# Performance work log

Measured on AMD Instinct MI355X. Metric: run time of the kernel, lower is better.

## Reference

```python
import jax, jax.numpy as jnp
import numpy as np

B, T, NMELS = 512, 180, 40
HID, NLAYER, PROJ = 768, 3, 256


def _lstm_layer(x, w_ih, w_hh, b):
    """PyTorch-convention LSTM layer. x: [B, T, D] -> h_seq: [B, T, H].
    Gate order i, f, g, o. b = b_ih + b_hh."""
    Bn = x.shape[0]
    H = w_hh.shape[1]
    # Input contribution for all timesteps at once: [T, B, 4H]
    xg = jnp.einsum('btd,gd->tbg', x, w_ih) + b

    def step(carry, xg_t):
        h, c = carry
        g = xg_t + h @ w_hh.T  # [B, 4H]
        i, f, gg, o = jnp.split(g, 4, axis=-1)
        i = jax.nn.sigmoid(i)
        f = jax.nn.sigmoid(f)
        gg = jnp.tanh(gg)
        o = jax.nn.sigmoid(o)
        c = f * c + i * gg
        h = o * jnp.tanh(c)
        return (h, c), h

    h0 = jnp.zeros((Bn, H), x.dtype)
    c0 = jnp.zeros((Bn, H), x.dtype)
    (_, _), hs = jax.lax.scan(step, (h0, c0), xg)  # hs: [T, B, H]
    return jnp.transpose(hs, (1, 0, 2))


def setup_inputs() -> dict:
    key = jax.random.key(0)
    ks = jax.random.split(key, 16)
    G = 4 * HID

    def xavier(k, shape):
        fan_out, fan_in = shape
        std = np.sqrt(2.0 / (fan_in + fan_out)).astype(np.float32)
        return jax.random.normal(k, shape, jnp.float32) * std

    inp = {
        'x': jax.random.normal(ks[0], (B, T, NMELS), jnp.float32),
        'w_ih0': xavier(ks[1], (G, NMELS)),
        'w_hh0': xavier(ks[2], (G, HID)),
        'b_ih0': jnp.zeros((G,), jnp.float32),
        'b_hh0': jnp.zeros((G,), jnp.float32),
        'w_ih1': xavier(ks[3], (G, HID)),
        'w_hh1': xavier(ks[4], (G, HID)),
        'b_ih1': jnp.zeros((G,), jnp.float32),
        'b_hh1': jnp.zeros((G,), jnp.float32),
        'w_ih2': xavier(ks[5], (G, HID)),
        'w_hh2': xavier(ks[6], (G, HID)),
        'b_ih2': jnp.zeros((G,), jnp.float32),
        'b_hh2': jnp.zeros((G,), jnp.float32),
        'proj_w': xavier(ks[7], (PROJ, HID)),
        'proj_b': jnp.zeros((PROJ,), jnp.float32),
    }
    return inp


def reference(x, w_ih0, w_hh0, b_ih0, b_hh0,
              w_ih1, w_hh1, b_ih1, b_hh1,
              w_ih2, w_hh2, b_ih2, b_hh2,
              proj_w, proj_b):
    h = _lstm_layer(x, w_ih0, w_hh0, b_ih0 + b_hh0)
    h = _lstm_layer(h, w_ih1, w_hh1, b_ih1 + b_hh1)
    h = _lstm_layer(h, w_ih2, w_hh2, b_ih2 + b_hh2)
    last = h[:, -1]                       # [B, HID] last timestep
    e = last @ proj_w.T + proj_b          # [B, PROJ]
    e = e / jnp.linalg.norm(e, axis=1, keepdims=True)
    return e
```

## Files before the change

kernel.cpp:

```cpp
#include <hip/hip_runtime.h>
#include <cstdint>
#include <cstddef>

using u16 = unsigned short;
using u32 = unsigned int;

typedef __attribute__((ext_vector_type(8)))  __bf16 bf16x8;
typedef __attribute__((ext_vector_type(16))) float  f32x16;

constexpr int kB   = 512;
constexpr int kT   = 180;
constexpr int kH   = 768;
constexpr int NBLK = 192;

constexpr int L0N  = 16 * 192 * 832;
constexpr int L12N = 16 * 192 * 1536;

constexpr int RING_SLOT_E = 24 * 512 * 32;
constexpr size_t RING_SZ  = (size_t)2 * RING_SLOT_E * 2;

constexpr size_t OFF_R0  = 256;
constexpr size_t OFF_R1  = OFF_R0 + RING_SZ;
constexpr size_t OFF_R2  = OFF_R1 + RING_SZ;
constexpr size_t OFF_PB  = OFF_R2 + RING_SZ;
constexpr size_t OFF_XT  = OFF_PB + (size_t)3 * 3072 * 4;
constexpr size_t OFF_W0  = OFF_XT + (size_t)kT * kB * 64 * 2;
constexpr size_t OFF_W1  = OFF_W0 + (size_t)L0N * 2;
constexpr size_t OFF_W2  = OFF_W1 + (size_t)L12N * 2;
constexpr size_t WS_NEED = OFF_W2 + (size_t)L12N * 2;

#define CLB __asm__ volatile("" ::: "memory")

__device__ __forceinline__ float bf2f(u16 u) {
  union { u32 i; float f; } v; v.i = ((u32)u) << 16; return v.f;
}
__device__ __forceinline__ u16 f2bf(float f) {
  union { float f; u32 i; } v; v.f = f;
  u32 r = v.i + 0x7fffu + ((v.i >> 16) & 1u);
  return (u16)(r >> 16);
}

typedef __attribute__((address_space(1))) const u32 as1_u32;
typedef __attribute__((address_space(3))) u32 as3_u32;
__device__ __forceinline__ void gload_lds16(const u16* g, u16* l) {
  __builtin_amdgcn_global_load_lds((as1_u32*)g, (as3_u32*)l, 16, 0, 0);
}
__device__ __forceinline__ void gload_lds16_dc(const u16* g, u16* l) {
  __builtin_amdgcn_global_load_lds((as1_u32*)g, (as3_u32*)l, 16, 0, 16);
}

__global__ void k_zero(uint4* p, int n) {
  uint4 z = make_uint4(0u, 0u, 0u, 0u);
  for (int i = blockIdx.x * 256 + threadIdx.x; i < n; i += gridDim.x * 256) p[i] = z;
}

__global__ void k_pack_w(const float* __restrict__ wih0, const float* __restrict__ whh0,
                         const float* __restrict__ wih1, const float* __restrict__ whh1,
                         const float* __restrict__ wih2, const float* __restrict__ whh2,
                         u16* __restrict__ W0, u16* __restrict__ W1, u16* __restrict__ W2) {
  int idx = blockIdx.x * 256 + threadIdx.x;
  if (idx < L0N) {
    int col = idx / 832, k = idx - col * 832;
    int ntile = col / 192, p = col - ntile * 192;
    int g = p / 48, hc = p - g * 48;
    int gcol = g * 768 + ntile * 48 + hc;
    float v = (k < 40) ? wih0[gcol * 40 + k]
                       : ((k < 64) ? 0.f : whh0[(size_t)gcol * 768 + (k - 64)]);
    W0[idx] = f2bf(v);
  } else if (idx < L0N + L12N) {
    int li = idx - L0N;
    int col = li / 1536, k = li - col * 1536;
    int ntile = col / 192, p = col - ntile * 192;
    int g = p / 48, hc = p - g * 48;
    int gcol = g * 768 + ntile * 48 + hc;
    float v = (k < 768) ? wih1[(size_t)gcol * 768 + k] : whh1[(size_t)gcol * 768 + (k - 768)];
    W1[li] = f2bf(v);
  } else {
    int li = idx - (L0N + L12N);
    if (li < L12N) {
      int col = li / 1536, k = li - col * 1536;
      int ntile = col / 192, p = col - ntile * 192;
      int g = p / 48, hc = p - g * 48;
      int gcol = g * 768 + ntile * 48 + hc;
      float v = (k < 768) ? wih2[(size_t)gcol * 768 + k] : whh2[(size_t)gcol * 768 + (k - 768)];
      W2[li] = f2bf(v);
    }
  }
}

__global__ void k_pack_b(const float* __restrict__ bi0, const float* __restrict__ bh0,
                         const float* __restrict__ bi1, const float* __restrict__ bh1,
                         const float* __restrict__ bi2, const float* __restrict__ bh2,
                         float* __restrict__ pbo) {
  int idx = blockIdx.x * 256 + threadIdx.x;
  int l = idx / 3072, r = idx - l * 3072;
  int ntile = r / 192, p = r - ntile * 192;
  int g = p / 48, hc = p - g * 48;
  int gcol = g * 768 + ntile * 48 + hc;
  const float* bi = (l == 0) ? bi0 : ((l == 1) ? bi1 : bi2);
  const float* bh = (l == 0) ? bh0 : ((l == 1) ? bh1 : bh2);
  pbo[idx] = bi[gcol] + bh[gcol];
}

__global__ void k_xT(const float* __restrict__ x, u16* __restrict__ xT) {
  int idx = blockIdx.x * 256 + threadIdx.x;
  int t = idx / (512 * 64);
  int r = idx - t * 512 * 64;
  int b = r >> 6, j = r & 63;
  float v = (j < 40) ? x[((size_t)b * 180 + t) * 40 + j] : 0.f;
  xT[(size_t)t * 32768 + (size_t)(j >> 5) * 16384 + b * 32 + (j & 31)] = f2bf(v);
}

__global__ __launch_bounds__(256, 2) void k_lstm(
    const u16* __restrict__ xT,
    u16* __restrict__ ring0, u16* __restrict__ ring1, u16* __restrict__ ring2,
    const u16* __restrict__ W0, const u16* __restrict__ W1, const u16* __restrict__ W2,
    const float* __restrict__ pb, u32* __restrict__ bar) {
  __shared__ __align__(16) unsigned char smem[61440 + 768];
  u16*   scr = (u16*)smem;
  float* pbs = (float*)(smem + 61440);

  const int tid = threadIdx.x;
  const int bid = blockIdx.x;
  const int xcd = bid & 7, j0 = bid >> 3;
  const int g_    = (j0 >> 2) * 8 + xcd;
  const int mt    = j0 & 3;
  const int layer = g_ >> 4;
  const int ntile = g_ & 15;
  const int mrow0 = mt * 128;

  const u16* Wl     = (layer == 0) ? W0 : ((layer == 1) ? W1 : W2);
  const int  Kl     = (layer == 0) ? 832 : 1536;
  const int  KcIn   = (layer == 0) ? 2 : 24;
  const int  nch    = (layer == 0) ? 26 : 48;
  const u16* inseq  = (layer == 1) ? ring0 : ring1;
  u16*       ringS  = (layer == 0) ? ring0 : ((layer == 1) ? ring1 : ring2);
  const u16* bbase0 = Wl + (size_t)(ntile * 192) * Kl;

  for (int i = tid; i < 192; i += 256) pbs[i] = pb[layer * 3072 + ntile * 192 + i];

  const int wid = tid >> 6, lane = tid & 63;
  const int wm = wid & 1, wn = wid >> 1;
  const int l31 = lane & 31, lhi = lane >> 5;

  float c_reg[24];
#pragma unroll
  for (int i = 0; i < 24; i++) c_reg[i] = 0.f;

  for (int s = 0; s < kT + 2; ++s) {
    const int t = s - layer;
    if (t >= 0 && t < kT) {
      f32x16 acc[2][3];
#pragma unroll
      for (int mi = 0; mi < 2; mi++)
#pragma unroll
        for (int ni = 0; ni < 3; ni++)
#pragma unroll
          for (int r = 0; r < 16; r++) acc[mi][ni][r] = 0.f;

      const u16* inbase  = (layer == 0) ? (xT + (size_t)t * 32768)
                                        : (inseq + (size_t)(t & 1) * RING_SLOT_E);
      const u16* recbase = ringS + (size_t)((t - 1) & 1) * RING_SLOT_E;

      auto stage = [&](int c, int st) {
        u16* sbA = (u16*)(smem + st * 20480);
        u16* sbB = sbA + 4096;
        const bool rsrc = (layer != 0) || (c >= KcIn);
        const u16* abase = (c < KcIn) ? (inbase + (size_t)c * 16384)
                                      : (recbase + (size_t)(c - KcIn) * 16384);
#pragma unroll
        for (int k = 0; k < 2; k++) {
          const int e = tid + k * 256;
          const int row = e >> 2, sp = e & 3;
          const int so = sp ^ ((row >> 1) & 3);
          const u16* ga = abase + (size_t)(mrow0 + row) * 32 + so * 8;
          u16*       la = sbA + (size_t)e * 8;
          if (rsrc) gload_lds16_dc(ga, la);
          else      gload_lds16(ga, la);
        }
        const u16* bb = bbase0 + c * 32;
#pragma unroll
        for (int k = 0; k < 3; k++) {
          const int e = tid + k * 256;
          const int col = e >> 2, sp = e & 3;
          const int so = sp ^ ((col >> 1) & 3);
          gload_lds16(bb + (size_t)col * Kl + so * 8, sbB + (size_t)e * 8);
        }
      };

      stage(0, 0);
      stage(1, 1);
      for (int c = 0; c < nch; ++c) {
        CLB;
        if (c == nch - 1) __builtin_amdgcn_s_waitcnt(0xF70);
        else              __builtin_amdgcn_s_waitcnt(0xF75);
        __builtin_amdgcn_s_barrier();
        CLB;
        if (c + 2 < nch) stage(c + 2, (c + 2) % 3);
        const u16* sA = (const u16*)(smem + (c % 3) * 20480);
        const u16* sB = sA + 4096;
        const int wsw = (l31 >> 1) & 3;
#pragma unroll
        for (int kk = 0; kk < 2; kk++) {
          const int sl = (((kk << 1) | lhi) ^ wsw) << 3;
          bf16x8 a0 = *(const bf16x8*)(sA + (wm * 64 +      l31) * 32 + sl);
          bf16x8 a1 = *(const bf16x8*)(sA + (wm * 64 + 32 + l31) * 32 + sl);
          const int c0 = wn * 96 + l31;
          bf16x8 b0 = *(const bf16x8*)(sB + (c0     ) * 32 + sl);
          bf16x8 b1 = *(const bf16x8*)(sB + (c0 + 32) * 32 + sl);
          bf16x8 b2 = *(const bf16x8*)(sB + (c0 + 64) * 32 + sl);
          acc[0][0] = __builtin_amdgcn_mfma_f32_32x32x16_bf16(a0, b0, acc[0][0], 0, 0, 0);
          acc[0][1] = __builtin_amdgcn_mfma_f32_32x32x16_bf16(a0, b1, acc[0][1], 0, 0, 0);
          acc[0][2] = __builtin_amdgcn_mfma_f32_32x32x16_bf16(a0, b2, acc[0][2], 0, 0, 0);
          acc[1][0] = __builtin_amdgcn_mfma_f32_32x32x16_bf16(a1, b0, acc[1][0], 0, 0, 0);
          acc[1][1] = __builtin_amdgcn_mfma_f32_32x32x16_bf16(a1, b1, acc[1][1], 0, 0, 0);
          acc[1][2] = __builtin_amdgcn_mfma_f32_32x32x16_bf16(a1, b2, acc[1][2], 0, 0, 0);
        }
      }
      __syncthreads();
#pragma unroll
      for (int mi = 0; mi < 2; mi++) {
#pragma unroll
        for (int ni = 0; ni < 3; ni++) {
          const int pcol = wn * 96 + ni * 32 + l31;
          const int gg = pcol / 48;
          const float bias = pbs[pcol];
#pragma unroll
          for (int r = 0; r < 16; r++) {
            const int rowl = wm * 64 + mi * 32 + (r & 3) + ((r >> 2) << 3) + (lhi << 2);
            float v = acc[mi][ni][r] + bias;
            v = (gg == 2) ? tanhf(v) : (1.f / (1.f + __expf(-v)));
            scr[rowl * 192 + pcol] = f2bf(v);
          }
        }
      }
      __syncthreads();
      u16* hout = ringS + (size_t)(t & 1) * RING_SLOT_E;
#pragma unroll
      for (int jj = 0; jj < 24; jj++) {
        const int idx = jj * 256 + tid;
        const int row = idx / 48;
        const int hc  = idx - row * 48;
        const float iv = bf2f(scr[row * 192       + hc]);
        const float fv = bf2f(scr[row * 192 +  48 + hc]);
        const float gv = bf2f(scr[row * 192 +  96 + hc]);
        const float ov = bf2f(scr[row * 192 + 144 + hc]);
        const float cn = fv * c_reg[jj] + iv * gv;
        c_reg[jj] = cn;
        const int colg = ntile * 48 + hc;
        hout[(size_t)(colg >> 5) * 16384 + (size_t)(mrow0 + row) * 32 + (colg & 31)]
            = f2bf(ov * tanhf(cn));
      }
    }
    __syncthreads();
    if (tid == 0) {
      __hip_atomic_fetch_add(bar, 1u, __ATOMIC_RELEASE, __HIP_MEMORY_SCOPE_AGENT);
      const u32 goal = (u32)(s + 1) * (u32)NBLK;
      u32 tries = 0;
      while (__hip_atomic_load(bar, __ATOMIC_RELAXED, __HIP_MEMORY_SCOPE_AGENT) < goal) {
        __builtin_amdgcn_s_sleep(8);
        if (++tries > 100000u) break;
      }
    }
    __syncthreads();
  }
}

__global__ __launch_bounds__(256) void k_proj(const u16* __restrict__ hlast,
                                              const float* __restrict__ pw,
                                              const float* __restrict__ pbv,
                                              float* __restrict__ out) {
  __shared__ float hs[8 * 768];
  __shared__ float wred[4 * 8];
  __shared__ float inv[8];
  const int tid = threadIdx.x;
  const int r0 = blockIdx.x * 8;
  for (int i = tid; i < 8 * 768; i += 256) {
    const int b = i / 768, col = i - b * 768;
    hs[i] = bf2f(hlast[(size_t)(col >> 5) * 16384 + (size_t)(r0 + b) * 32 + (col & 31)]);
  }
  __syncthreads();
  float acc[8];
#pragma unroll
  for (int r = 0; r < 8; r++) acc[r] = 0.f;
  const float* wrow = pw + (size_t)tid * 768;
  for (int k = 0; k < 768; k++) {
    float w = wrow[k];
#pragma unroll
    for (int r = 0; r < 8; r++) acc[r] += hs[r * 768 + k] * w;
  }
  const float bv = pbv[tid];
#pragma unroll
  for (int r = 0; r < 8; r++) acc[r] += bv;
  const int lane = tid & 63, w4 = tid >> 6;
#pragma unroll
  for (int r = 0; r < 8; r++) {
    float v = acc[r] * acc[r];
#pragma unroll
    for (int off = 32; off > 0; off >>= 1) v += __shfl_xor(v, off);
    if (lane == 0) wred[w4 * 8 + r] = v;
  }
  __syncthreads();
  if (tid < 8) {
    float sum = wred[tid] + wred[8 + tid] + wred[16 + tid] + wred[24 + tid];
    inv[tid] = 1.f / sqrtf(sum);
  }
  __syncthreads();
#pragma unroll
  for (int r = 0; r < 8; r++) out[(size_t)(r0 + r) * 256 + tid] = acc[r] * inv[r];
}

extern "C" void kernel_launch(void* const* d_in, const int* in_sizes, int n_in,
                              void* d_out, int out_size, void* d_ws, size_t ws_size,
                              hipStream_t stream) {
  const float* x    = (const float*)d_in[0];
  const float* wih0 = (const float*)d_in[1];
  const float* whh0 = (const float*)d_in[2];
  const float* bi0  = (const float*)d_in[3];
  const float* bh0  = (const float*)d_in[4];
  const float* wih1 = (const float*)d_in[5];
  const float* whh1 = (const float*)d_in[6];
  const float* bi1  = (const float*)d_in[7];
  const float* bh1  = (const float*)d_in[8];
  const float* wih2 = (const float*)d_in[9];
  const float* whh2 = (const float*)d_in[10];
  const float* bi2  = (const float*)d_in[11];
  const float* bh2  = (const float*)d_in[12];
  const float* pw   = (const float*)d_in[13];
  const float* pbv  = (const float*)d_in[14];

  if (ws_size < WS_NEED) return;

  char* ws  = (char*)d_ws;
  u32*  bar = (u32*)(ws + 0);
  u16*  r0  = (u16*)(ws + OFF_R0);
  u16*  r1  = (u16*)(ws + OFF_R1);
  u16*  r2  = (u16*)(ws + OFF_R2);
  float* pb = (float*)(ws + OFF_PB);
  u16*  xT  = (u16*)(ws + OFF_XT);
  u16*  W0  = (u16*)(ws + OFF_W0);
  u16*  W1  = (u16*)(ws + OFF_W1);
  u16*  W2  = (u16*)(ws + OFF_W2);

  hipLaunchKernelGGL(k_zero, dim3(512), dim3(256), 0, stream,
                     (uint4*)ws, (int)(OFF_PB / 16));
  hipLaunchKernelGGL(k_pack_w, dim3((L0N + 2 * L12N + 255) / 256), dim3(256), 0, stream,
                     wih0, whh0, wih1, whh1, wih2, whh2, W0, W1, W2);
  hipLaunchKernelGGL(k_pack_b, dim3(36), dim3(256), 0, stream,
                     bi0, bh0, bi1, bh1, bi2, bh2, pb);
  hipLaunchKernelGGL(k_xT, dim3(kT * kB * 64 / 256), dim3(256), 0, stream, x, xT);

  {
    const u16* xTc = xT; const float* pbc = pb;
    const u16 *W0c = W0, *W1c = W1, *W2c = W2;
    u16 *r0m = r0, *r1m = r1, *r2m = r2; u32* barm = bar;
    void* kargs[] = {(void*)&xTc, (void*)&r0m, (void*)&r1m, (void*)&r2m,
                     (void*)&W0c, (void*)&W1c, (void*)&W2c, (void*)&pbc, (void*)&barm};
    hipLaunchCooperativeKernel((void*)k_lstm, dim3(NBLK), dim3(256), kargs, 0, stream);
  }

  hipLaunchKernelGGL(k_proj, dim3(64), dim3(256), 0, stream,
                     r2 + (size_t)((kT - 1) & 1) * RING_SLOT_E, pw, pbv, (float*)d_out);
}
```

Measured before the change: 9.341 ms.

## Replace global grid barrier with per-row-tile dataflow flags and wider blocks

Halves the block count to 96 with 512 threads each, so every block now computes a 384-column gate tile and the weights are repacked to match. The single grid-wide barrier per step is replaced by per-(layer, row-tile) counters. Each block waits only on its input layer, its own previous step and the next layer's consumption of the ring slot. The LDS pipeline moves to four dynamic-shared-memory stages of 32 KB, and biases are held in registers. The aim is to cut global barrier latency and let layers run in a wavefront, at the cost of more LDS per block, fewer blocks and subtler ordering correctness.

Measured after the change: 9.980 ms. 6.8% more time.

```diff
diff --git a/kernel.cpp b/kernel.cpp
--- a/kernel.cpp
+++ b/kernel.cpp
@@ -11,15 +11,16 @@
 constexpr int kB   = 512;
 constexpr int kT   = 180;
 constexpr int kH   = 768;
-constexpr int NBLK = 192;
-
-constexpr int L0N  = 16 * 192 * 832;
-constexpr int L12N = 16 * 192 * 1536;
+constexpr int NBLK = 96;
+constexpr int NTHR = 512;
+
+constexpr int L0N  = 8 * 384 * 832;
+constexpr int L12N = 8 * 384 * 1536;
 
 constexpr int RING_SLOT_E = 24 * 512 * 32;
 constexpr size_t RING_SZ  = (size_t)2 * RING_SLOT_E * 2;
 
-constexpr size_t OFF_R0  = 256;
+constexpr size_t OFF_R0  = 4096;
 constexpr size_t OFF_R1  = OFF_R0 + RING_SZ;
 constexpr size_t OFF_R2  = OFF_R1 + RING_SZ;
 constexpr size_t OFF_PB  = OFF_R2 + RING_SZ;
@@ -29,6 +30,10 @@
 constexpr size_t OFF_W2  = OFF_W1 + (size_t)L12N * 2;
 constexpr size_t WS_NEED = OFF_W2 + (size_t)L12N * 2;
 
+constexpr size_t STAGE_SZ = 32768;
+constexpr int    NSTG     = 4;
+constexpr size_t DYN_LDS  = NSTG * STAGE_SZ;
+
 #define CLB __asm__ volatile("" ::: "memory")
 
 __device__ __forceinline__ float bf2f(u16 u) {
@@ -61,27 +66,27 @@
   int idx = blockIdx.x * 256 + threadIdx.x;
   if (idx < L0N) {
     int col = idx / 832, k = idx - col * 832;
-    int ntile = col / 192, p = col - ntile * 192;
-    int g = p / 48, hc = p - g * 48;
-    int gcol = g * 768 + ntile * 48 + hc;
+    int ntile = col / 384, p = col - ntile * 384;
+    int g = p / 96, hc = p - g * 96;
+    int gcol = g * 768 + ntile * 96 + hc;
     float v = (k < 40) ? wih0[gcol * 40 + k]
                        : ((k < 64) ? 0.f : whh0[(size_t)gcol * 768 + (k - 64)]);
     W0[idx] = f2bf(v);
   } else if (idx < L0N + L12N) {
     int li = idx - L0N;
     int col = li / 1536, k = li - col * 1536;
-    int ntile = col / 192, p = col - ntile * 192;
-    int g = p / 48, hc = p - g * 48;
-    int gcol = g * 768 + ntile * 48 + hc;
+    int ntile = col / 384, p = col - ntile * 384;
+    int g = p / 96, hc = p - g * 96;
+    int gcol = g * 768 + ntile * 96 + hc;
     float v = (k < 768) ? wih1[(size_t)gcol * 768 + k] : whh1[(size_t)gcol * 768 + (k - 768)];
     W1[li] = f2bf(v);
   } else {
     int li = idx - (L0N + L12N);
     if (li < L12N) {
       int col = li / 1536, k = li - col * 1536;
-      int ntile = col / 192, p = col - ntile * 192;
-      int g = p / 48, hc = p - g * 48;
-      int gcol = g * 768 + ntile * 48 + hc;
+      int ntile = col / 384, p = col - ntile * 384;
+      int g = p / 96, hc = p - g * 96;
+      int gcol = g * 768 + ntile * 96 + hc;
       float v = (k < 768) ? wih2[(size_t)gcol * 768 + k] : whh2[(size_t)gcol * 768 + (k - 768)];
       W2[li] = f2bf(v);
     }
@@ -94,9 +99,9 @@
                          float* __restrict__ pbo) {
   int idx = blockIdx.x * 256 + threadIdx.x;
   int l = idx / 3072, r = idx - l * 3072;
-  int ntile = r / 192, p = r - ntile * 192;
-  int g = p / 48, hc = p - g * 48;
-  int gcol = g * 768 + ntile * 48 + hc;
+  int ntile = r / 384, p = r - ntile * 384;
+  int g = p / 96, hc = p - g * 96;
+  int gcol = g * 768 + ntile * 96 + hc;
   const float* bi = (l == 0) ? bi0 : ((l == 1) ? bi1 : bi2);
   const float* bh = (l == 0) ? bh0 : ((l == 1) ? bh1 : bh2);
   pbo[idx] = bi[gcol] + bh[gcol];
@@ -111,22 +116,20 @@
   xT[(size_t)t * 32768 + (size_t)(j >> 5) * 16384 + b * 32 + (j & 31)] = f2bf(v);
 }
 
-__global__ __launch_bounds__(256, 2) void k_lstm(
+__global__ __launch_bounds__(512, 2) void k_lstm(
     const u16* __restrict__ xT,
     u16* __restrict__ ring0, u16* __restrict__ ring1, u16* __restrict__ ring2,
     const u16* __restrict__ W0, const u16* __restrict__ W1, const u16* __restrict__ W2,
-    const float* __restrict__ pb, u32* __restrict__ bar) {
-  __shared__ __align__(16) unsigned char smem[61440 + 768];
-  u16*   scr = (u16*)smem;
-  float* pbs = (float*)(smem + 61440);
+    const float* __restrict__ pb, u32* __restrict__ flg) {
+  extern __shared__ __align__(16) unsigned char smem[];
+  u16* scr = (u16*)smem;
 
   const int tid = threadIdx.x;
   const int bid = blockIdx.x;
-  const int xcd = bid & 7, j0 = bid >> 3;
-  const int g_    = (j0 >> 2) * 8 + xcd;
+  const int ntile = bid & 7;
+  const int j0    = bid >> 3;
+  const int layer = j0 >> 2;
   const int mt    = j0 & 3;
-  const int layer = g_ >> 4;
-  const int ntile = g_ & 15;
   const int mrow0 = mt * 128;
 
   const u16* Wl     = (layer == 0) ? W0 : ((layer == 1) ? W1 : W2);
@@ -135,134 +138,145 @@
   const int  nch    = (layer == 0) ? 26 : 48;
   const u16* inseq  = (layer == 1) ? ring0 : ring1;
   u16*       ringS  = (layer == 0) ? ring0 : ((layer == 1) ? ring1 : ring2);
-  const u16* bbase0 = Wl + (size_t)(ntile * 192) * Kl;
-
-  for (int i = tid; i < 192; i += 256) pbs[i] = pb[layer * 3072 + ntile * 192 + i];
+  const u16* bbase0 = Wl + (size_t)(ntile * 384) * Kl;
+
+  u32* Fself = flg + (size_t)((layer * 4 + mt) * 64);
+  u32* Fin   = flg + (size_t)(((layer - 1) * 4 + mt) * 64);
+  u32* Fnxt  = flg + (size_t)(((layer + 1) * 4 + mt) * 64);
 
   const int wid = tid >> 6, lane = tid & 63;
   const int wm = wid & 1, wn = wid >> 1;
   const int l31 = lane & 31, lhi = lane >> 5;
 
+  float bias_r[3];
+#pragma unroll
+  for (int ni = 0; ni < 3; ni++)
+    bias_r[ni] = pb[layer * 3072 + ntile * 384 + wn * 96 + ni * 32 + l31];
+
   float c_reg[24];
 #pragma unroll
   for (int i = 0; i < 24; i++) c_reg[i] = 0.f;
 
-  for (int s = 0; s < kT + 2; ++s) {
-    const int t = s - layer;
-    if (t >= 0 && t < kT) {
-      f32x16 acc[2][3];
-#pragma unroll
-      for (int mi = 0; mi < 2; mi++)
-#pragma unroll
-        for (int ni = 0; ni < 3; ni++)
-#pragma unroll
-          for (int r = 0; r < 16; r++) acc[mi][ni][r] = 0.f;
-
-      const u16* inbase  = (layer == 0) ? (xT + (size_t)t * 32768)
-                                        : (inseq + (size_t)(t & 1) * RING_SLOT_E);
-      const u16* recbase = ringS + (size_t)((t - 1) & 1) * RING_SLOT_E;
-
-      auto stage = [&](int c, int st) {
-        u16* sbA = (u16*)(smem + st * 20480);
-        u16* sbB = sbA + 4096;
-        const bool rsrc = (layer != 0) || (c >= KcIn);
-        const u16* abase = (c < KcIn) ? (inbase + (size_t)c * 16384)
-                                      : (recbase + (size_t)(c - KcIn) * 16384);
-#pragma unroll
-        for (int k = 0; k < 2; k++) {
-          const int e = tid + k * 256;
-          const int row = e >> 2, sp = e & 3;
-          const int so = sp ^ ((row >> 1) & 3);
-          const u16* ga = abase + (size_t)(mrow0 + row) * 32 + so * 8;
-          u16*       la = sbA + (size_t)e * 8;
-          if (rsrc) gload_lds16_dc(ga, la);
-          else      gload_lds16(ga, la);
-        }
-        const u16* bb = bbase0 + c * 32;
-#pragma unroll
-        for (int k = 0; k < 3; k++) {
-          const int e = tid + k * 256;
-          const int col = e >> 2, sp = e & 3;
-          const int so = sp ^ ((col >> 1) & 3);
-          gload_lds16(bb + (size_t)col * Kl + so * 8, sbB + (size_t)e * 8);
+  for (int t = 0; t < kT; ++t) {
+    if (tid == 0) {
+      auto spinf = [&](u32* f, u32 goal) {
+        u32 tries = 0;
+        while (__hip_atomic_load(f, __ATOMIC_RELAXED, __HIP_MEMORY_SCOPE_AGENT) < goal) {
+          __builtin_amdgcn_s_sleep(4);
+          if (++tries > 400000u) break;
         }
       };
-
-      stage(0, 0);
-      stage(1, 1);
-      for (int c = 0; c < nch; ++c) {
-        CLB;
-        if (c == nch - 1) __builtin_amdgcn_s_waitcnt(0xF70);
-        else              __builtin_amdgcn_s_waitcnt(0xF75);
-        __builtin_amdgcn_s_barrier();
-        CLB;
-        if (c + 2 < nch) stage(c + 2, (c + 2) % 3);
-        const u16* sA = (const u16*)(smem + (c % 3) * 20480);
-        const u16* sB = sA + 4096;
-        const int wsw = (l31 >> 1) & 3;
-#pragma unroll
-        for (int kk = 0; kk < 2; kk++) {
-          const int sl = (((kk << 1) | lhi) ^ wsw) << 3;
-          bf16x8 a0 = *(const bf16x8*)(sA + (wm * 64 +      l31) * 32 + sl);
-          bf16x8 a1 = *(const bf16x8*)(sA + (wm * 64 + 32 + l31) * 32 + sl);
-          const int c0 = wn * 96 + l31;
-          bf16x8 b0 = *(const bf16x8*)(sB + (c0     ) * 32 + sl);
-          bf16x8 b1 = *(const bf16x8*)(sB + (c0 + 32) * 32 + sl);
-          bf16x8 b2 = *(const bf16x8*)(sB + (c0 + 64) * 32 + sl);
-          acc[0][0] = __builtin_amdgcn_mfma_f32_32x32x16_bf16(a0, b0, acc[0][0], 0, 0, 0);
-          acc[0][1] = __builtin_amdgcn_mfma_f32_32x32x16_bf16(a0, b1, acc[0][1], 0, 0, 0);
-          acc[0][2] = __builtin_amdgcn_mfma_f32_32x32x16_bf16(a0, b2, acc[0][2], 0, 0, 0);
-          acc[1][0] = __builtin_amdgcn_mfma_f32_32x32x16_bf16(a1, b0, acc[1][0], 0, 0, 0);
-          acc[1][1] = __builtin_amdgcn_mfma_f32_32x32x16_bf16(a1, b1, acc[1][1], 0, 0, 0);
-          acc[1][2] = __builtin_amdgcn_mfma_f32_32x32x16_bf16(a1, b2, acc[1][2], 0, 0, 0);
+      if (layer >= 1)           spinf(Fin,   8u * (u32)(t + 1));
+      if (t >= 1)               spinf(Fself, 8u * (u32)t);
+      if (layer <= 1 && t >= 2) spinf(Fnxt,  8u * (u32)(t - 1));
+    }
+    __syncthreads();
+
+    f32x16 acc[2][3];
+#pragma unroll
+    for (int mi = 0; mi < 2; mi++)
+#pragma unroll
+      for (int ni = 0; ni < 3; ni++)
+#pragma unroll
+        for (int r = 0; r < 16; r++) acc[mi][ni][r] = 0.f;
+
+    const u16* inbase  = (layer == 0) ? (xT + (size_t)t * 32768)
+                                      : (inseq + (size_t)(t & 1) * RING_SLOT_E);
+    const u16* recbase = ringS + (size_t)((t - 1) & 1) * RING_SLOT_E;
+
+    auto stage = [&](int c, int st) {
+      u16* sbA = (u16*)(smem + (size_t)st * STAGE_SZ);
+      u16* sbB = sbA + 4096;
+      const bool rsrc = (layer != 0) || (c >= KcIn);
+      const u16* abase = (c < KcIn) ? (inbase + (size_t)c * 16384)
+                                    : (recbase + (size_t)(c - KcIn) * 16384);
+      {
+        const int e = tid;
+        const int row = e >> 2, sp = e & 3;
+        const int so = sp ^ ((row >> 1) & 3);
+        const u16* ga = abase + (size_t)(mrow0 + row) * 32 + so * 8;
+        u16*       la = sbA + (size_t)e * 8;
+        if (rsrc) gload_lds16_dc(ga, la);
+        else      gload_lds16(ga, la);
+      }
+      const u16* bb = bbase0 + c * 32;
+#pragma unroll
+      for (int k = 0; k < 3; k++) {
+        const int e = tid + k * 512;
+        const int col = e >> 2, sp = e & 3;
+        const int so = sp ^ ((col >> 1) & 3);
+        gload_lds16(bb + (size_t)col * Kl + so * 8, sbB + (size_t)e * 8);
+      }
+    };
+
+    stage(0, 0);
+    stage(1, 1);
+    stage(2, 2);
+    for (int c = 0; c < nch; ++c) {
+      CLB;
+      const int rem = nch - 1 - c;
+      if      (rem >= 2) __builtin_amdgcn_s_waitcnt(0x0F78);
+      else if (rem == 1) __builtin_amdgcn_s_waitcnt(0x0F74);
+      else               __builtin_amdgcn_s_waitcnt(0x0F70);
+      __builtin_amdgcn_s_barrier();
+      CLB;
+      if (c + 3 < nch) stage(c + 3, (c + 3) & 3);
+      const u16* sA = (const u16*)(smem + (size_t)(c & 3) * STAGE_SZ);
+      const u16* sB = sA + 4096;
+      const int wsw = (l31 >> 1) & 3;
+#pragma unroll
+      for (int kk = 0; kk < 2; kk++) {
+        const int sl = (((kk << 1) | lhi) ^ wsw) << 3;
+        bf16x8 a0 = *(const bf16x8*)(sA + (wm * 64 +      l31) * 32 + sl);
+        bf16x8 a1 = *(const bf16x8*)(sA + (wm * 64 + 32 + l31) * 32 + sl);
+        const int c0 = wn * 96 + l31;
+        bf16x8 b0 = *(const bf16x8*)(sB + (c0     ) * 32 + sl);
+        bf16x8 b1 = *(const bf16x8*)(sB + (c0 + 32) * 32 + sl);
+        bf16x8 b2 = *(const bf16x8*)(sB + (c0 + 64) * 32 + sl);
+        acc[0][0] = __builtin_amdgcn_mfma_f32_32x32x16_bf16(a0, b0, acc[0][0], 0, 0, 0);
+        acc[0][1] = __builtin_amdgcn_mfma_f32_32x32x16_bf16(a0, b1, acc[0][1], 0, 0, 0);
+        acc[0][2] = __builtin_amdgcn_mfma_f32_32x32x16_bf16(a0, b2, acc[0][2], 0, 0, 0);
+        acc[1][0] = __builtin_amdgcn_mfma_f32_32x32x16_bf16(a1, b0, acc[1][0], 0, 0, 0);
+        acc[1][1] = __builtin_amdgcn_mfma_f32_32x32x16_bf16(a1, b1, acc[1][1], 0, 0, 0);
+        acc[1][2] = __builtin_amdgcn_mfma_f32_32x32x16_bf16(a1, b2, acc[1][2], 0, 0, 0);
+      }
+    }
+    __syncthreads();
+#pragma unroll
+    for (int mi = 0; mi < 2; mi++) {
+#pragma unroll
+      for (int ni = 0; ni < 3; ni++) {
+        const int pcol = wn * 96 + ni * 32 + l31;
+        const float bias = bias_r[ni];
+#pragma unroll
+        for (int r = 0; r < 16; r++) {
+          const int rowl = wm * 64 + mi * 32 + (r & 3) + ((r >> 2) << 3) + (lhi << 2);
+          float v = acc[mi][ni][r] + bias;
+          v = (wn == 2) ? tanhf(v) : (1.f / (1.f + __expf(-v)));
+          scr[rowl * 384 + pcol] = f2bf(v);
         }
       }
-      __syncthreads();
-#pragma unroll
-      for (int mi = 0; mi < 2; mi++) {
-#pragma unroll
-        for (int ni = 0; ni < 3; ni++) {
-          const int pcol = wn * 96 + ni * 32 + l31;
-          const int gg = pcol / 48;
-          const float bias = pbs[pcol];
-#pragma unroll
-          for (int r = 0; r < 16; r++) {
-            const int rowl = wm * 64 + mi * 32 + (r & 3) + ((r >> 2) << 3) + (lhi << 2);
-            float v = acc[mi][ni][r] + bias;
-            v = (gg == 2) ? tanhf(v) : (1.f / (1.f + __expf(-v)));
-            scr[rowl * 192 + pcol] = f2bf(v);
-          }
-        }
-      }
-      __syncthreads();
-      u16* hout = ringS + (size_t)(t & 1) * RING_SLOT_E;
-#pragma unroll
-      for (int jj = 0; jj < 24; jj++) {
-        const int idx = jj * 256 + tid;
-        const int row = idx / 48;
-        const int hc  = idx - row * 48;
-        const float iv = bf2f(scr[row * 192       + hc]);
-        const float fv = bf2f(scr[row * 192 +  48 + hc]);
-        const float gv = bf2f(scr[row * 192 +  96 + hc]);
-        const float ov = bf2f(scr[row * 192 + 144 + hc]);
-        const float cn = fv * c_reg[jj] + iv * gv;
-        c_reg[jj] = cn;
-        const int colg = ntile * 48 + hc;
-        hout[(size_t)(colg >> 5) * 16384 + (size_t)(mrow0 + row) * 32 + (colg & 31)]
-            = f2bf(ov * tanhf(cn));
-      }
     }
     __syncthreads();
-    if (tid == 0) {
-      __hip_atomic_fetch_add(bar, 1u, __ATOMIC_RELEASE, __HIP_MEMORY_SCOPE_AGENT);
-      const u32 goal = (u32)(s + 1) * (u32)NBLK;
-      u32 tries = 0;
-      while (__hip_atomic_load(bar, __ATOMIC_RELAXED, __HIP_MEMORY_SCOPE_AGENT) < goal) {
-        __builtin_amdgcn_s_sleep(8);
-        if (++tries > 100000u) break;
-      }
+    u16* hout = ringS + (size_t)(t & 1) * RING_SLOT_E;
+#pragma unroll
+    for (int jj = 0; jj < 24; jj++) {
+      const int idx = jj * 512 + tid;
+      const int row = idx / 96;
+      const int hc  = idx - row * 96;
+      const float iv = bf2f(scr[row * 384       + hc]);
+      const float fv = bf2f(scr[row * 384 +  96 + hc]);
+      const float gv = bf2f(scr[row * 384 + 192 + hc]);
+      const float ov = bf2f(scr[row * 384 + 288 + hc]);
+      const float cn = fv * c_reg[jj] + iv * gv;
+      c_reg[jj] = cn;
+      const int colg = ntile * 96 + hc;
+      hout[(size_t)(colg >> 5) * 16384 + (size_t)(mrow0 + row) * 32 + (colg & 31)]
+          = f2bf(ov * tanhf(cn));
     }
     __syncthreads();
+    if (tid == 0)
+      __hip_atomic_fetch_add(Fself, 1u, __ATOMIC_RELEASE, __HIP_MEMORY_SCOPE_AGENT);
   }
 }
 
@@ -331,8 +345,16 @@
 
   if (ws_size < WS_NEED) return;
 
+  static bool attr_done = false;
+  if (!attr_done) {
+    (void)hipFuncSetAttribute((const void*)k_lstm,
+                              hipFuncAttributeMaxDynamicSharedMemorySize,
+                              (int)DYN_LDS);
+    attr_done = true;
+  }
+
   char* ws  = (char*)d_ws;
-  u32*  bar = (u32*)(ws + 0);
+  u32*  flg = (u32*)(ws + 0);
   u16*  r0  = (u16*)(ws + OFF_R0);
   u16*  r1  = (u16*)(ws + OFF_R1);
   u16*  r2  = (u16*)(ws + OFF_R2);
@@ -353,10 +375,11 @@
   {
     const u16* xTc = xT; const float* pbc = pb;
     const u16 *W0c = W0, *W1c = W1, *W2c = W2;
-    u16 *r0m = r0, *r1m = r1, *r2m = r2; u32* barm = bar;
+    u16 *r0m = r0, *r1m = r1, *r2m = r2; u32* flgm = flg;
     void* kargs[] = {(void*)&xTc, (void*)&r0m, (void*)&r1m, (void*)&r2m,
-                     (void*)&W0c, (void*)&W1c, (void*)&W2c, (void*)&pbc, (void*)&barm};
-    hipLaunchCooperativeKernel((void*)k_lstm, dim3(NBLK), dim3(256), kargs, 0, stream);
+                     (void*)&W0c, (void*)&W1c, (void*)&W2c, (void*)&pbc, (void*)&flgm};
+    hipLaunchCooperativeKernel((void*)k_lstm, dim3(NBLK), dim3(NTHR), kargs,
+                               (unsigned int)DYN_LDS, stream);
   }
 
   hipLaunchKernelGGL(k_proj, dim3(64), dim3(256), 0, stream,
```

## Add row-sliced LSTM kernel with per-group flags replacing global grid barrier

Applied to the files above, without the earlier changes.

Adds a new persistent LSTM kernel using 256 blocks. Each block owns a 32-row batch slice and one gate tile, is pinned to its XCD through the hardware XCC id, and runs all three layers in sequence. The single global barrier per wavefront step is replaced by per-slice, per-layer counters, so only the 16 blocks that share rows wait on each other, and layers can pipeline across timesteps. The K loop uses a 6-stage LDS pipeline with split-K across waves and an LDS reduction. The old kernel is kept as a fallback when the device has fewer than 256 CUs or the launch fails. The risks are more serial layer work per block and the extra overhead of flag spinning.

Result: no change. 9.382 ms (+0.4%).

```diff
diff --git a/kernel.cpp b/kernel.cpp
--- a/kernel.cpp
+++ b/kernel.cpp
@@ -11,7 +11,8 @@
 constexpr int kB   = 512;
 constexpr int kT   = 180;
 constexpr int kH   = 768;
-constexpr int NBLK = 192;
+constexpr int NBLK_RS = 256;
+constexpr int NBLK_FB = 192;
 
 constexpr int L0N  = 16 * 192 * 832;
 constexpr int L12N = 16 * 192 * 1536;
@@ -19,7 +20,7 @@
 constexpr int RING_SLOT_E = 24 * 512 * 32;
 constexpr size_t RING_SZ  = (size_t)2 * RING_SLOT_E * 2;
 
-constexpr size_t OFF_R0  = 256;
+constexpr size_t OFF_R0  = 16384;
 constexpr size_t OFF_R1  = OFF_R0 + RING_SZ;
 constexpr size_t OFF_R2  = OFF_R1 + RING_SZ;
 constexpr size_t OFF_PB  = OFF_R2 + RING_SZ;
@@ -29,6 +30,10 @@
 constexpr size_t OFF_W2  = OFF_W1 + (size_t)L12N * 2;
 constexpr size_t WS_NEED = OFF_W2 + (size_t)L12N * 2;
 
+constexpr size_t STAGE_SZ = 14336;
+constexpr int    NSTG     = 6;
+constexpr size_t DYN_LDS  = NSTG * STAGE_SZ;
+
 #define CLB __asm__ volatile("" ::: "memory")
 
 __device__ __forceinline__ float bf2f(u16 u) {
@@ -44,6 +49,9 @@
 typedef __attribute__((address_space(3))) u32 as3_u32;
 __device__ __forceinline__ void gload_lds16(const u16* g, u16* l) {
   __builtin_amdgcn_global_load_lds((as1_u32*)g, (as3_u32*)l, 16, 0, 0);
+}
+__device__ __forceinline__ void gload_lds16_l2(const u16* g, u16* l) {
+  __builtin_amdgcn_global_load_lds((as1_u32*)g, (as3_u32*)l, 16, 0, 1);
 }
 __device__ __forceinline__ void gload_lds16_dc(const u16* g, u16* l) {
   __builtin_amdgcn_global_load_lds((as1_u32*)g, (as3_u32*)l, 16, 0, 16);
@@ -111,7 +119,198 @@
   xT[(size_t)t * 32768 + (size_t)(j >> 5) * 16384 + b * 32 + (j & 31)] = f2bf(v);
 }
 
-__global__ __launch_bounds__(256, 2) void k_lstm(
+__global__ __launch_bounds__(256, 1) void k_lstm_rs(
+    const u16* __restrict__ xT,
+    u16* __restrict__ ring0, u16* __restrict__ ring1, u16* __restrict__ ring2,
+    const u16* __restrict__ W0, const u16* __restrict__ W1, const u16* __restrict__ W2,
+    const float* __restrict__ pb, u32* __restrict__ flg) {
+  extern __shared__ __align__(16) unsigned char smem[];
+  float* red  = (float*)smem;
+  u16*   scr2 = (u16*)(smem + 24576);
+  __shared__ u32 meta[2];
+
+  const int tid = threadIdx.x;
+  if (tid == 0) {
+    u32 xcc;
+    asm volatile("s_getreg_b32 %0, hwreg(HW_REG_XCC_ID)" : "=s"(xcc));
+    xcc &= 7u;
+    u32* xcnt = flg + 3072;
+    u32 slot = __hip_atomic_fetch_add(&xcnt[xcc], 1u, __ATOMIC_RELAXED,
+                                      __HIP_MEMORY_SCOPE_AGENT);
+    meta[0] = xcc; meta[1] = slot & 31u;
+  }
+  __syncthreads();
+  const int xcc = (int)meta[0];
+  const int rs  = (int)(meta[1] >> 4);
+  const int nt  = (int)(meta[1] & 15u);
+  const int r0  = xcc * 64 + rs * 32;
+
+  const int wid = tid >> 6, lane = tid & 63;
+  const int wn2 = wid & 1, kkw = wid >> 1;
+  const int l31 = lane & 31, lhi = lane >> 5;
+
+  u32* F0 = flg + (size_t)(((xcc * 2 + rs) * 3 + 0) * 64);
+  u32* F1 = F0 + 64;
+  u32* F2 = F0 + 128;
+
+  auto spinf = [&](u32* f, u32 goal) {
+    u32 tries = 0;
+    while (__hip_atomic_load(f, __ATOMIC_RELAXED, __HIP_MEMORY_SCOPE_AGENT) < goal) {
+      __builtin_amdgcn_s_sleep(4);
+      if (++tries > 400000u) break;
+    }
+  };
+
+  float bias_r[3][3];
+#pragma unroll
+  for (int l = 0; l < 3; l++)
+#pragma unroll
+    for (int j = 0; j < 3; j++)
+      bias_r[l][j] = pb[l * 3072 + nt * 192 + wn2 * 96 + j * 32 + l31];
+
+  float cst[3][6];
+#pragma unroll
+  for (int l = 0; l < 3; l++)
+#pragma unroll
+    for (int j = 0; j < 6; j++) cst[l][j] = 0.f;
+
+  for (int t = 0; t < kT; ++t) {
+#pragma unroll
+    for (int l = 0; l < 3; ++l) {
+      const u16* Wl   = (l == 0) ? W0 : ((l == 1) ? W1 : W2);
+      const int  Kl   = (l == 0) ? 832 : 1536;
+      const int  KcIn = (l == 0) ? 2 : 24;
+      const int  nch  = (l == 0) ? 26 : 48;
+      u16* ringL = (l == 0) ? ring0 : ((l == 1) ? ring1 : ring2);
+      const u16* inb  = (l == 0) ? (xT + (size_t)t * 32768)
+                                 : (((l == 1) ? ring0 : ring1) + (size_t)(t & 1) * RING_SLOT_E);
+      const u16* recb = ringL + (size_t)((t - 1) & 1) * RING_SLOT_E;
+      const u16* bb0  = Wl + (size_t)(nt * 192) * Kl;
+      u32* Fl = (l == 0) ? F0 : ((l == 1) ? F1 : F2);
+
+      if (tid == 0) {
+        if (l == 0) {
+          if (t >= 1) spinf(F0, 16u * (u32)t);
+          if (t >= 2) spinf(F1, 16u * (u32)(t - 1));
+        } else if (l == 1) {
+          spinf(F0, 16u * (u32)(t + 1));
+          if (t >= 1) spinf(F1, 16u * (u32)t);
+          if (t >= 2) spinf(F2, 16u * (u32)(t - 1));
+        } else {
+          spinf(F1, 16u * (u32)(t + 1));
+          if (t >= 1) spinf(F2, 16u * (u32)t);
+        }
+      }
+      __syncthreads();
+
+      f32x16 acc[3];
+#pragma unroll
+      for (int j = 0; j < 3; j++)
+#pragma unroll
+        for (int r = 0; r < 16; r++) acc[j][r] = 0.f;
+
+      auto stage = [&](int c, int st) {
+        u16* sbA = (u16*)(smem + (size_t)st * STAGE_SZ);
+        u16* sbB = sbA + 1024;
+        const bool rsrc = (l != 0) || (c >= KcIn);
+        const u16* abase = (c < KcIn) ? (inb + (size_t)c * 16384)
+                                      : (recb + (size_t)(c - KcIn) * 16384);
+        if (lane < 32) {
+          const int e = (wid << 5) | lane;
+          const int row = e >> 2, sp = e & 3;
+          const int so = sp ^ ((row >> 1) & 3);
+          const u16* ga = abase + (size_t)(r0 + row) * 32 + so * 8;
+          u16*       la = sbA + (size_t)e * 8;
+          if (rsrc) gload_lds16_l2(ga, la);
+          else      gload_lds16(ga, la);
+        }
+        const u16* bb = bb0 + c * 32;
+#pragma unroll
+        for (int k = 0; k < 3; k++) {
+          const int e = wid * 192 + (k << 6) + lane;
+          const int col = e >> 2, sp = e & 3;
+          const int so = sp ^ ((col >> 1) & 3);
+          gload_lds16(bb + (size_t)col * Kl + so * 8, sbB + (size_t)e * 8);
+        }
+      };
+
+      stage(0, 0); stage(1, 1); stage(2, 2); stage(3, 3); stage(4, 4);
+      for (int c = 0; c < nch; ++c) {
+        CLB;
+        const int rem = nch - 1 - c;
+        switch (rem > 3 ? 4 : rem) {
+          case 0:  __builtin_amdgcn_s_waitcnt(0x0F70); break;
+          case 1:  __builtin_amdgcn_s_waitcnt(0x0F74); break;
+          case 2:  __builtin_amdgcn_s_waitcnt(0x0F78); break;
+          case 3:  __builtin_amdgcn_s_waitcnt(0x0F7C); break;
+          default: __builtin_amdgcn_s_waitcnt(0x4F70); break;
+        }
+        __builtin_amdgcn_s_barrier();
+        CLB;
+        if (c + 5 < nch) stage(c + 5, (c + 5) % NSTG);
+        const u16* sA = (const u16*)(smem + (size_t)(c % NSTG) * STAGE_SZ);
+        const u16* sB = sA + 1024;
+        const int wsw = (l31 >> 1) & 3;
+        const int sl = (((kkw << 1) | lhi) ^ wsw) << 3;
+        bf16x8 a  = *(const bf16x8*)(sA + l31 * 32 + sl);
+        const int c0 = wn2 * 96 + l31;
+        bf16x8 b0 = *(const bf16x8*)(sB + (c0     ) * 32 + sl);
+        bf16x8 b1 = *(const bf16x8*)(sB + (c0 + 32) * 32 + sl);
+        bf16x8 b2 = *(const bf16x8*)(sB + (c0 + 64) * 32 + sl);
+        acc[0] = __builtin_amdgcn_mfma_f32_32x32x16_bf16(a, b0, acc[0], 0, 0, 0);
+        acc[1] = __builtin_amdgcn_mfma_f32_32x32x16_bf16(a, b1, acc[1], 0, 0, 0);
+        acc[2] = __builtin_amdgcn_mfma_f32_32x32x16_bf16(a, b2, acc[2], 0, 0, 0);
+      }
+      __syncthreads();
+
+      if (kkw == 1) {
+#pragma unroll
+        for (int j = 0; j < 3; j++)
+#pragma unroll
+          for (int r = 0; r < 16; r++)
+            red[(size_t)((wn2 * 3 + j) * 16 + r) * 64 + lane] = acc[j][r];
+      }
+      __syncthreads();
+      if (kkw == 0) {
+#pragma unroll
+        for (int j = 0; j < 3; j++) {
+          const int pcol = wn2 * 96 + j * 32 + l31;
+          const int gate = pcol / 48;
+          const float bias = bias_r[l][j];
+#pragma unroll
+          for (int r = 0; r < 16; r++) {
+            const int rowl = (r & 3) + ((r >> 2) << 3) + (lhi << 2);
+            float v = acc[j][r] + red[(size_t)((wn2 * 3 + j) * 16 + r) * 64 + lane] + bias;
+            v = (gate == 2) ? tanhf(v) : (1.f / (1.f + __expf(-v)));
+            scr2[rowl * 192 + pcol] = f2bf(v);
+          }
+        }
+      }
+      __syncthreads();
+      u16* hout = ringL + (size_t)(t & 1) * RING_SLOT_E;
+#pragma unroll
+      for (int jj = 0; jj < 6; jj++) {
+        const int idx = jj * 256 + tid;
+        const int row = idx / 48;
+        const int hc  = idx - row * 48;
+        const float iv = bf2f(scr2[row * 192       + hc]);
+        const float fv = bf2f(scr2[row * 192 +  48 + hc]);
+        const float gv = bf2f(scr2[row * 192 +  96 + hc]);
+        const float ov = bf2f(scr2[row * 192 + 144 + hc]);
+        const float cn = fv * cst[l][jj] + iv * gv;
+        cst[l][jj] = cn;
+        const int colg = nt * 48 + hc;
+        hout[(size_t)(colg >> 5) * 16384 + (size_t)(r0 + row) * 32 + (colg & 31)]
+            = f2bf(ov * tanhf(cn));
+      }
+      __syncthreads();
+      if (tid == 0)
+        __hip_atomic_fetch_add(Fl, 1u, __ATOMIC_RELEASE, __HIP_MEMORY_SCOPE_AGENT);
+    }
+  }
+}
+
+__global__ __launch_bounds__(256, 2) void k_lstm_fb(
     const u16* __restrict__ xT,
     u16* __restrict__ ring0, u16* __restrict__ ring1, u16* __restrict__ ring2,
     const u16* __restrict__ W0, const u16* __restrict__ W1, const u16* __restrict__ W2,
@@ -255,7 +454,7 @@
     __syncthreads();
     if (tid == 0) {
       __hip_atomic_fetch_add(bar, 1u, __ATOMIC_RELEASE, __HIP_MEMORY_SCOPE_AGENT);
-      const u32 goal = (u32)(s + 1) * (u32)NBLK;
+      const u32 goal = (u32)(s + 1) * (u32)NBLK_FB;
       u32 tries = 0;
       while (__hip_atomic_load(bar, __ATOMIC_RELAXED, __HIP_MEMORY_SCOPE_AGENT) < goal) {
         __builtin_amdgcn_s_sleep(8);
@@ -331,8 +530,24 @@
 
   if (ws_size < WS_NEED) return;
 
+  static int mode = -1;
+  if (mode < 0) {
+    hipError_t e1 = hipFuncSetAttribute((const void*)k_lstm_rs,
+                                        hipFuncAttributeMaxDynamicSharedMemorySize,
+                                        (int)DYN_LDS);
+    int nb = 0;
+    hipError_t e2 = hipOccupancyMaxActiveBlocksPerMultiprocessor(
+        &nb, k_lstm_rs, 256, (size_t)DYN_LDS);
+    int dev = 0; hipGetDevice(&dev);
+    hipDeviceProp_t props{};
+    hipError_t e3 = hipGetDeviceProperties(&props, dev);
+    mode = (e1 == hipSuccess && e2 == hipSuccess && e3 == hipSuccess &&
+            nb >= 1 && props.multiProcessorCount >= NBLK_RS) ? 1 : 0;
+  }
+
   char* ws  = (char*)d_ws;
-  u32*  bar = (u32*)(ws + 0);
+  u32*  flg = (u32*)(ws + 0);
+  u32*  bar = flg + 3200;
   u16*  r0  = (u16*)(ws + OFF_R0);
   u16*  r1  = (u16*)(ws + OFF_R1);
   u16*  r2  = (u16*)(ws + OFF_R2);
@@ -353,10 +568,22 @@
   {
     const u16* xTc = xT; const float* pbc = pb;
     const u16 *W0c = W0, *W1c = W1, *W2c = W2;
-    u16 *r0m = r0, *r1m = r1, *r2m = r2; u32* barm = bar;
-    void* kargs[] = {(void*)&xTc, (void*)&r0m, (void*)&r1m, (void*)&r2m,
-                     (void*)&W0c, (void*)&W1c, (void*)&W2c, (void*)&pbc, (void*)&barm};
-    hipLaunchCooperativeKernel((void*)k_lstm, dim3(NBLK), dim3(256), kargs, 0, stream);
+    u16 *r0m = r0, *r1m = r1, *r2m = r2;
+    u32* flgm = flg; u32* barm = bar;
+    void* kargs_rs[] = {(void*)&xTc, (void*)&r0m, (void*)&r1m, (void*)&r2m,
+                        (void*)&W0c, (void*)&W1c, (void*)&W2c, (void*)&pbc, (void*)&flgm};
+    void* kargs_fb[] = {(void*)&xTc, (void*)&r0m, (void*)&r1m, (void*)&r2m,
+                        (void*)&W0c, (void*)&W1c, (void*)&W2c, (void*)&pbc, (void*)&barm};
+    if (mode == 1) {
+      hipError_t le = hipLaunchCooperativeKernel((void*)k_lstm_rs, dim3(NBLK_RS),
+                                                 dim3(256), kargs_rs,
+                                                 (unsigned int)DYN_LDS, stream);
+      if (le != hipSuccess) mode = 0;
+    }
+    if (mode == 0) {
+      hipLaunchCooperativeKernel((void*)k_lstm_fb, dim3(NBLK_FB), dim3(256),
+                                 kargs_fb, 0, stream);
+    }
   }
 
   hipLaunchKernelGGL(k_proj, dim3(64), dim3(256), 0, stream,
```
